# Kernel tuning notes

Hardware: AMD Instinct MI355X
Metric: run time of the kernel (lower is better)

Reference implementation:

```python
import jax, jax.numpy as jnp
import numpy as np

B, Q, HID = 2, 2048, 2048
HQ, HKV, D = 16, 4, 128
EPS = 1e-6
THETA = 1000000.0


def _rmsnorm(x, w):
    # x: [..., D]
    return x * jax.lax.rsqrt(jnp.mean(x * x, axis=-1, keepdims=True) + EPS) * w


def _rope(x, cos, sin):
    # neox-style: split halves. x: [B,Q,H,D], cos/sin: [B,Q,1,D/2]
    d2 = x.shape[-1] // 2
    x1, x2 = x[..., :d2], x[..., d2:]
    return jnp.concatenate([x1 * cos - x2 * sin, x2 * cos + x1 * sin], axis=-1)


def setup_inputs() -> dict:
    key = jax.random.key(0)
    k1, k2, k3 = jax.random.split(key, 3)
    positions = jnp.broadcast_to(jnp.arange(Q, dtype=jnp.int32), (B, Q))
    hidden_states = jax.random.normal(k1, (B, Q, HID), dtype=jnp.float32)
    k_cache = jnp.zeros((B, HKV, Q, D), dtype=jnp.float32)
    v_cache = jnp.zeros((B, HKV, Q, D), dtype=jnp.float32)
    wqkv = jax.random.normal(k2, (HQ * D + 2 * HKV * D, HID), dtype=jnp.float32) * (HID ** -0.5)
    wo = jax.random.normal(k3, (HID, HQ * D), dtype=jnp.float32) * ((HQ * D) ** -0.5)
    q_norm_w = jnp.ones((D,), dtype=jnp.float32)
    k_norm_w = jnp.ones((D,), dtype=jnp.float32)
    return {"positions": positions, "hidden_states": hidden_states, "k_cache": k_cache,
            "v_cache": v_cache, "wqkv": wqkv, "wo": wo, "q_norm_w": q_norm_w,
            "k_norm_w": k_norm_w, "seq_len": Q}


def reference(positions, hidden_states, k_cache, v_cache, wqkv, wo, q_norm_w, k_norm_w, seq_len):
    bsz, qlen, _ = hidden_states.shape
    q_size, kv_size = HQ * D, HKV * D
    scale = D ** -0.5

    qkv = hidden_states.reshape(bsz * qlen, HID) @ wqkv.T  # [B*Q, q+2kv]
    q = qkv[:, :q_size].reshape(bsz, qlen, HQ, D)
    k = qkv[:, q_size:q_size + kv_size].reshape(bsz, qlen, HKV, D)
    v = qkv[:, q_size + kv_size:].reshape(bsz, qlen, HKV, D)

    q = _rmsnorm(q, q_norm_w)
    k = _rmsnorm(k, k_norm_w)

    inv_freq = 1.0 / (THETA ** (jnp.arange(0, D, 2, dtype=jnp.float32) / D))  # [D/2]
    freqs = positions.astype(jnp.float32)[..., None] * inv_freq  # [B,Q,D/2]
    cos = jnp.cos(freqs)[:, :, None, :]
    sin = jnp.sin(freqs)[:, :, None, :]
    q = _rope(q, cos, sin)
    k = _rope(k, cos, sin)

    q = q.transpose(0, 2, 1, 3)  # [B,HQ,Q,D]
    k = k.transpose(0, 2, 1, 3)  # [B,HKV,Q,D]
    v = v.transpose(0, 2, 1, 3)

    start = seq_len - qlen
    k_cache = jax.lax.dynamic_update_slice(k_cache, k, (0, 0, start, 0))
    v_cache = jax.lax.dynamic_update_slice(v_cache, v, (0, 0, start, 0))
    k_full = k_cache[:, :, :seq_len, :]
    v_full = v_cache[:, :, :seq_len, :]

    rep = HQ // HKV
    kf = jnp.repeat(k_full, rep, axis=1)  # [B,HQ,S,D]
    vf = jnp.repeat(v_full, rep, axis=1)

    scores = jnp.einsum('bhqd,bhkd->bhqk', q, kf) * scale
    if qlen == seq_len:  # is_causal path
        causal = jnp.tril(jnp.ones((qlen, seq_len), dtype=bool))
        scores = jnp.where(causal, scores, jnp.finfo(scores.dtype).min)
    attn = jax.nn.softmax(scores, axis=-1)
    out = jnp.einsum('bhqk,bhkd->bhqd', attn, vf)  # [B,HQ,Q,D]
    out = out.transpose(0, 2, 1, 3).reshape(bsz * qlen, HQ * D)
    return (out @ wo.T).reshape(bsz, qlen, HID)
```

## Files before the change

### kernel.cpp

```cpp
#include <hip/hip_runtime.h>

#define B_    2
#define Q_    2048
#define HID_  2048
#define HQ_   16
#define HKV_  4
#define D_    128
#define QSC_  (0.08838834764831843f * 1.4426950408889634f)
#define LOG2_THETA 19.931568569324174f
#define FMAX_ 20.0f

typedef unsigned short u16;
typedef __attribute__((ext_vector_type(8))) short bf16x8;
typedef __attribute__((ext_vector_type(4))) float f32x4;

__device__ __forceinline__ u16 f2bf(float x) {
  union { float f; unsigned int u; } v; v.f = x;
  unsigned int r = v.u + 0x7FFFu + ((v.u >> 16) & 1u);
  return (u16)(r >> 16);
}
__device__ __forceinline__ u16 f2bf_t(float x) {
  union { float f; unsigned int u; } v; v.f = x;
  return (u16)(v.u >> 16);
}

__device__ __forceinline__ void gl2lds16(u16* lds, const u16* g) {
  __builtin_amdgcn_global_load_lds((const __attribute__((address_space(1))) void*)g,
                                   (__attribute__((address_space(3))) void*)lds,
                                   16, 0, 0);
}

#define N4_HID  2097152
#define N4_WQKV 1572864
#define N4_WO   1048576
#define N4_ALL  (N4_HID + N4_WQKV + N4_WO)
#define NROPE   (B_ * Q_ * 64)
__global__ __launch_bounds__(256) void cvt_all(const float* __restrict__ h,
                                               const float* __restrict__ wq,
                                               const float* __restrict__ wo,
                                               const int* __restrict__ pos,
                                               u16* __restrict__ oh,
                                               u16* __restrict__ owq,
                                               u16* __restrict__ owo,
                                               float* __restrict__ rope) {
  int i = blockIdx.x * 256 + threadIdx.x;
  if (i >= N4_ALL) {
    int j = i - N4_ALL;
    int d = j & 63, row = j >> 6;
    float p = (float)pos[row];
    float inv = exp2f(-(float)d * (LOG2_THETA / 64.f));
    float sn, cn;
    sincosf(p * inv, &sn, &cn);
    ((float2*)rope)[j] = make_float2(cn, sn);
    return;
  }
  const float* src; u16* dst; int off;
  if (i < N4_HID)                 { src = h;  dst = oh;  off = i; }
  else if (i < N4_HID + N4_WQKV)  { src = wq; dst = owq; off = i - N4_HID; }
  else                            { src = wo; dst = owo; off = i - N4_HID - N4_WQKV; }
  float4 v = *(const float4*)(src + (size_t)off * 4);
  ushort4 o;
  o.x = f2bf(v.x); o.y = f2bf(v.y); o.z = f2bf(v.z); o.w = f2bf(v.w);
  *(ushort4*)(dst + (size_t)off * 4) = o;
}

__global__ __launch_bounds__(256) void gemm_qkv(const u16* __restrict__ A,
                                                const u16* __restrict__ Bw,
                                                const float* __restrict__ rope,
                                                const float* __restrict__ qw,
                                                const float* __restrict__ kw,
                                                u16* __restrict__ qb,
                                                u16* __restrict__ kb,
                                                u16* __restrict__ vt) {
  __shared__ __align__(16) u16 lds[12288];
  u16* As = lds;
  u16* Bs = lds + 4096;
  const int tid = threadIdx.x;
  const int wv = tid >> 6, lane = tid & 63;
  const int c = lane & 15, quad = lane >> 4;
  const int lr = lane >> 2, lp = lane & 3;
  const int lpg = (lp + 4 - ((lr >> 1) & 3)) & 3;
  const int swq = ((quad + (c >> 1)) & 3) * 8;
  const int m0 = blockIdx.x * 128;
  const int by = blockIdx.y;
  const int n0 = by * 128;
  f32x4 acc[2][8] = {};
  for (int k0 = 0; k0 < HID_; k0 += 32) {
    __syncthreads();
#pragma unroll
    for (int i = 0; i < 2; i++) {
      int r = wv * 16 + i * 64 + lr;
      gl2lds16(As + (size_t)(wv * 64 + i * 256) * 8,
               A + (size_t)(m0 + r) * HID_ + k0 + lpg * 8);
      gl2lds16(Bs + (size_t)(wv * 64 + i * 256) * 8,
               Bw + (size_t)(n0 + r) * HID_ + k0 + lpg * 8);
    }
    __syncthreads();
    bf16x8 af[2], bfr[8];
#pragma unroll
    for (int mi = 0; mi < 2; mi++)
      af[mi] = *(const bf16x8*)(As + (wv * 32 + mi * 16 + c) * 32 + swq);
#pragma unroll
    for (int ni = 0; ni < 8; ni++)
      bfr[ni] = *(const bf16x8*)(Bs + (ni * 16 + c) * 32 + swq);
#pragma unroll
    for (int mi = 0; mi < 2; mi++)
#pragma unroll
      for (int ni = 0; ni < 8; ni++)
        acc[mi][ni] = __builtin_amdgcn_mfma_f32_16x16x32_bf16(af[mi], bfr[ni],
                                                              acc[mi][ni], 0, 0, 0);
  }
  __syncthreads();

  if (by < 20) {
    const bool isq = by < 16;
    const float* w = isq ? qw : kw;
    const float osc = isq ? QSC_ : 1.f;
    float wl[8];
#pragma unroll
    for (int ni = 0; ni < 8; ni++) wl[ni] = w[ni * 16 + c];
    u16* dstbuf = isq ? qb : kb;
    const int hbase = isq ? by : (by - 16);
    const int nheads = isq ? HQ_ : HKV_;
#pragma unroll
    for (int ph = 0; ph < 2; ph++) {
      if (ph) __syncthreads();
      if ((wv >> 1) == ph) {
#pragma unroll
        for (int mi = 0; mi < 2; mi++)
#pragma unroll
          for (int r = 0; r < 4; r++) {
            const int row = m0 + wv * 32 + mi * 16 + quad * 4 + r;
            const int q = row & (Q_ - 1), b = row >> 11;
            float ss = 0.f;
#pragma unroll
            for (int ni = 0; ni < 8; ni++) ss += acc[mi][ni][r] * acc[mi][ni][r];
            ss += __shfl_xor(ss, 1); ss += __shfl_xor(ss, 2);
            ss += __shfl_xor(ss, 4); ss += __shfl_xor(ss, 8);
            const float rn = rsqrtf(ss * (1.f / 128.f) + 1e-6f) * osc;
            u16* lrow = lds + ((wv & 1) * 32 + mi * 16 + quad * 4 + r) * 132;
#pragma unroll
            for (int ni = 0; ni < 4; ni++) {
              float2 cssn = *(const float2*)(rope +
                  ((size_t)(b * Q_ + q) * 64 + ni * 16 + c) * 2);
              float x1 = acc[mi][ni][r]     * wl[ni]     * rn;
              float x2 = acc[mi][ni + 4][r] * wl[ni + 4] * rn;
              lrow[ni * 16 + c]       = f2bf(x1 * cssn.x - x2 * cssn.y);
              lrow[(ni + 4) * 16 + c] = f2bf(x2 * cssn.x + x1 * cssn.y);
            }
          }
      }
      __syncthreads();
      const int rowg = m0 + ph * 64 + (tid >> 2);
      const int q = rowg & (Q_ - 1), b = rowg >> 11;
      u16* dst = dstbuf + (((size_t)(b * nheads) + hbase) * Q_ + q) * D_ + (tid & 3) * 32;
      const u16* srcl = lds + (tid >> 2) * 132 + (tid & 3) * 32;
#pragma unroll
      for (int j = 0; j < 4; j++)
        *(bf16x8*)(dst + j * 8) = *(const bf16x8*)(srcl + j * 8);
    }
  } else {
    const int hk = by - 20;
    const int bb = m0 >> 11, q0 = m0 & (Q_ - 1);
    u16* vw = lds + wv * 3072;
#pragma unroll
    for (int mi = 0; mi < 2; mi++) {
      if (mi) __syncthreads();
#pragma unroll
      for (int ni = 0; ni < 8; ni++) {
        short4 pv;
        pv.x = (short)f2bf(acc[mi][ni][0]); pv.y = (short)f2bf(acc[mi][ni][1]);
        pv.z = (short)f2bf(acc[mi][ni][2]); pv.w = (short)f2bf(acc[mi][ni][3]);
        *(short4*)(vw + (ni * 16 + c) * 24 + quad * 4) = pv;
      }
      __syncthreads();
#pragma unroll
      for (int it = 0; it < 2; it++) {
        const int d = it * 64 + lane;
        const u16* src = vw + d * 24;
        u16* dst = vt + (((size_t)(bb * HKV_) + hk) * D_ + d) * Q_ +
                   q0 + wv * 32 + mi * 16;
        *(bf16x8*)(dst)     = *(const bf16x8*)(src);
        *(bf16x8*)(dst + 8) = *(const bf16x8*)(src + 8);
      }
    }
  }
}

__global__ __launch_bounds__(256) void gemm_bt(const u16* __restrict__ A,
                                               const u16* __restrict__ Bw,
                                               float* __restrict__ C,
                                               int M, int N, int K) {
  __shared__ __align__(16) u16 As[128 * 32];
  __shared__ __align__(16) u16 Bs[128 * 32];
  const int tid = threadIdx.x;
  const int wave = tid >> 6, lane = tid & 63;
  const int wm = wave & 1, wn = wave >> 1;
  const int row16 = lane & 15, quad = lane >> 4;
  const int lr = lane >> 2, lp = lane & 3;
  const int lpg = (lp + 4 - ((lr >> 1) & 3)) & 3;
  const int swq = ((quad + (row16 >> 1)) & 3) * 8;
  const int m0 = blockIdx.x * 128, n0 = blockIdx.y * 128;
  f32x4 acc[4][4] = {};
  for (int k0 = 0; k0 < K; k0 += 32) {
    __syncthreads();
#pragma unroll
    for (int i = 0; i < 2; i++) {
      int r = wave * 16 + i * 64 + lr;
      gl2lds16(As + (size_t)(wave * 64 + i * 256) * 8,
               A + (size_t)(m0 + r) * K + k0 + lpg * 8);
      gl2lds16(Bs + (size_t)(wave * 64 + i * 256) * 8,
               Bw + (size_t)(n0 + r) * K + k0 + lpg * 8);
    }
    __syncthreads();
    bf16x8 af[4], bfr[4];
#pragma unroll
    for (int t = 0; t < 4; t++) {
      af[t]  = *(const bf16x8*)(As + (wm * 64 + t * 16 + row16) * 32 + swq);
      bfr[t] = *(const bf16x8*)(Bs + (wn * 64 + t * 16 + row16) * 32 + swq);
    }
#pragma unroll
    for (int mi = 0; mi < 4; mi++)
#pragma unroll
      for (int ni = 0; ni < 4; ni++)
        acc[mi][ni] = __builtin_amdgcn_mfma_f32_16x16x32_bf16(af[mi], bfr[ni],
                                                              acc[mi][ni], 0, 0, 0);
  }
#pragma unroll
  for (int mi = 0; mi < 4; mi++) {
    int row = m0 + wm * 64 + mi * 16 + quad * 4;
#pragma unroll
    for (int ni = 0; ni < 4; ni++) {
      int col = n0 + wn * 64 + ni * 16 + row16;
#pragma unroll
      for (int r = 0; r < 4; r++)
        C[(size_t)(row + r) * N + col] = acc[mi][ni][r];
    }
  }
}

__global__ __launch_bounds__(256) void attn_fwd(const u16* __restrict__ qb,
                                                const u16* __restrict__ kb,
                                                const u16* __restrict__ vt,
                                                u16* __restrict__ ob) {
  __shared__ __align__(16) u16 lds[8192 + 8192 + 4608];
  u16* Ks = lds;
  u16* Vs = lds + 8192;
  u16* Ps = lds + 16384;
  const int p = blockIdx.x, h = blockIdx.y, b = blockIdx.z;
  const int hk = h >> 2;
  const int tid = threadIdx.x, wave = tid >> 6, lane = tid & 63;
  const int c = lane & 15, quad = lane >> 4;
  const int lr = lane >> 2, lp = lane & 3;
  const int lpg = (lp + 4 - ((lr >> 1) & 3)) & 3;
  const int swq = ((quad + (c >> 1)) & 3) * 8;
  const u16* qg = qb + ((size_t)b * HQ_ + h) * (size_t)Q_ * D_;
  const u16* kg = kb + ((size_t)b * HKV_ + hk) * (size_t)Q_ * D_;
  const u16* vg = vt + ((size_t)b * HKV_ + hk) * (size_t)D_ * Q_;
  u16* Pw = Ps + wave * 1152;
  u16* Bw = Ks + wave * 2176;

#pragma unroll 1
  for (int tp = 0; tp < 2; tp++) {
    const int t = tp ? (31 - p) : p;
    const int q0 = t * 64;
    const int qrow = q0 + wave * 16 + c;
    bf16x8 qf[4];
#pragma unroll
    for (int kk = 0; kk < 4; kk++)
      qf[kk] = *(const bf16x8*)(qg + (size_t)qrow * D_ + kk * 32 + quad * 8);
    f32x4 Oa[8] = {};
    float l_acc = 0.f;

#pragma unroll 1
    for (int kt = 0; kt <= t; kt++) {
      __syncthreads();
#pragma unroll
      for (int i = 0; i < 4; i++) {
        gl2lds16(Ks + (size_t)(i * 256 + wave * 64) * 8,
                 kg + ((size_t)kt * 64 + wave * 16 + lr) * D_ + i * 32 + lpg * 8);
        int d = (i & 1) * 64 + wave * 16 + lr;
        gl2lds16(Vs + (size_t)(i * 256 + wave * 64) * 8,
                 vg + (size_t)d * Q_ + kt * 64 + (i >> 1) * 32 + lpg * 8);
      }
      __syncthreads();
      f32x4 S[4];
#pragma unroll
      for (int n = 0; n < 4; n++) {
        f32x4 a = {-FMAX_, -FMAX_, -FMAX_, -FMAX_};
#pragma unroll
        for (int kk = 0; kk < 4; kk++) {
          bf16x8 kf = *(const bf16x8*)(Ks + kk * 2048 + (n * 16 + c) * 32 + swq);
          a = __builtin_amdgcn_mfma_f32_16x16x32_bf16(kf, qf[kk], a, 0, 0, 0);
        }
        S[n] = a;
      }
      if (kt == t) {
#pragma unroll
        for (int n = 0; n < 4; n++)
#pragma unroll
          for (int r = 0; r < 4; r++) {
            int key = kt * 64 + n * 16 + quad * 4 + r;
            if (key > qrow) S[n][r] = -1e9f;
          }
      }
#pragma unroll
      for (int n = 0; n < 4; n++) {
        float p0 = __builtin_amdgcn_exp2f(S[n][0]);
        float p1 = __builtin_amdgcn_exp2f(S[n][1]);
        float p2 = __builtin_amdgcn_exp2f(S[n][2]);
        float p3 = __builtin_amdgcn_exp2f(S[n][3]);
        l_acc += (p0 + p1) + (p2 + p3);
        short4 pk;
        pk.x = (short)f2bf_t(p0); pk.y = (short)f2bf_t(p1);
        pk.z = (short)f2bf_t(p2); pk.w = (short)f2bf_t(p3);
        *(short4*)(Pw + c * 72 + n * 16 + quad * 4) = pk;
      }
      bf16x8 pf[2];
#pragma unroll
      for (int kk2 = 0; kk2 < 2; kk2++)
        pf[kk2] = *(const bf16x8*)(Pw + c * 72 + kk2 * 32 + quad * 8);
#pragma unroll
      for (int md = 0; md < 8; md++)
#pragma unroll
        for (int kk2 = 0; kk2 < 2; kk2++) {
          bf16x8 vf = *(const bf16x8*)(Vs + kk2 * 4096 + (md * 16 + c) * 32 + swq);
          Oa[md] = __builtin_amdgcn_mfma_f32_16x16x32_bf16(vf, pf[kk2], Oa[md], 0, 0, 0);
        }
    }
    float l_row = l_acc;
    l_row += __shfl_xor(l_row, 16);
    l_row += __shfl_xor(l_row, 32);
    __syncthreads();
    const float invl = 1.f / l_row;
#pragma unroll
    for (int md = 0; md < 8; md++) {
      short4 ok;
      ok.x = (short)f2bf(Oa[md][0] * invl); ok.y = (short)f2bf(Oa[md][1] * invl);
      ok.z = (short)f2bf(Oa[md][2] * invl); ok.w = (short)f2bf(Oa[md][3] * invl);
      *(short4*)(Bw + c * 136 + md * 16 + quad * 4) = ok;
    }
    const int orow = q0 + wave * 16 + lr;
#pragma unroll
    for (int tt = 0; tt < 4; tt++) {
      bf16x8 ov = *(const bf16x8*)(Bw + lr * 136 + lp * 32 + tt * 8);
      *(bf16x8*)(ob + ((size_t)(b * Q_ + orow) * HQ_ + h) * D_ + lp * 32 + tt * 8) = ov;
    }
  }
}

extern "C" void kernel_launch(void* const* d_in, const int* in_sizes, int n_in,
                              void* d_out, int out_size, void* d_ws, size_t ws_size,
                              hipStream_t stream) {
  const int*   positions = (const int*)  d_in[0];
  const float* hidden    = (const float*)d_in[1];
  const float* wqkv      = (const float*)d_in[4];
  const float* wo        = (const float*)d_in[5];
  const float* qnw       = (const float*)d_in[6];
  const float* knw       = (const float*)d_in[7];
  char* ws = (char*)d_ws;
  u16*   hid_bf  = (u16*)(ws);
  u16*   wqkv_bf = (u16*)(ws + 16777216);
  u16*   wo_bf   = (u16*)(ws + 29360128);
  u16*   q_bf    = (u16*)(ws + 37748736);
  u16*   k_bf    = (u16*)(ws + 54525952);
  u16*   vt_bf   = (u16*)(ws + 58720256);
  float* rope    = (float*)(ws + 62914560);
  u16*   attn_bf = hid_bf;

  cvt_all<<<19456, 256, 0, stream>>>(hidden, wqkv, wo, positions,
                                     hid_bf, wqkv_bf, wo_bf, rope);
  gemm_qkv<<<dim3(32, 24), 256, 0, stream>>>(hid_bf, wqkv_bf, rope, qnw, knw,
                                             q_bf, k_bf, vt_bf);
  attn_fwd<<<dim3(16, 16, 2), 256, 0, stream>>>(q_bf, k_bf, vt_bf, attn_bf);
  gemm_bt<<<dim3(32, 16), 256, 0, stream>>>(attn_bf, wo_bf, (float*)d_out, 4096, 2048, 2048);
}
```

Measured before the change: 338.9 us.

## Rewrite output projection GEMM with 256x256 tiles and pipelined LDS staging

```diff
diff --git a/kernel.cpp b/kernel.cpp
--- a/kernel.cpp
+++ b/kernel.cpp
@@ -187,56 +187,195 @@
   }
 }
 
-__global__ __launch_bounds__(256) void gemm_bt(const u16* __restrict__ A,
-                                               const u16* __restrict__ Bw,
-                                               float* __restrict__ C,
-                                               int M, int N, int K) {
-  __shared__ __align__(16) u16 As[128 * 32];
-  __shared__ __align__(16) u16 Bs[128 * 32];
+__global__ __launch_bounds__(512) void gemm_bt8(const u16* __restrict__ A,
+                                                const u16* __restrict__ Bw,
+                                                float* __restrict__ C,
+                                                int M, int N, int K) {
+  __shared__ __align__(16) u16 lds[65536];
   const int tid = threadIdx.x;
-  const int wave = tid >> 6, lane = tid & 63;
-  const int wm = wave & 1, wn = wave >> 1;
-  const int row16 = lane & 15, quad = lane >> 4;
-  const int lr = lane >> 2, lp = lane & 3;
-  const int lpg = (lp + 4 - ((lr >> 1) & 3)) & 3;
-  const int swq = ((quad + (row16 >> 1)) & 3) * 8;
-  const int m0 = blockIdx.x * 128, n0 = blockIdx.y * 128;
-  f32x4 acc[4][4] = {};
-  for (int k0 = 0; k0 < K; k0 += 32) {
-    __syncthreads();
-#pragma unroll
-    for (int i = 0; i < 2; i++) {
-      int r = wave * 16 + i * 64 + lr;
-      gl2lds16(As + (size_t)(wave * 64 + i * 256) * 8,
-               A + (size_t)(m0 + r) * K + k0 + lpg * 8);
-      gl2lds16(Bs + (size_t)(wave * 64 + i * 256) * 8,
-               Bw + (size_t)(n0 + r) * K + k0 + lpg * 8);
-    }
-    __syncthreads();
-    bf16x8 af[4], bfr[4];
-#pragma unroll
-    for (int t = 0; t < 4; t++) {
-      af[t]  = *(const bf16x8*)(As + (wm * 64 + t * 16 + row16) * 32 + swq);
-      bfr[t] = *(const bf16x8*)(Bs + (wn * 64 + t * 16 + row16) * 32 + swq);
-    }
-#pragma unroll
-    for (int mi = 0; mi < 4; mi++)
-#pragma unroll
-      for (int ni = 0; ni < 4; ni++)
-        acc[mi][ni] = __builtin_amdgcn_mfma_f32_16x16x32_bf16(af[mi], bfr[ni],
-                                                              acc[mi][ni], 0, 0, 0);
+  const int wv = tid >> 6, lane = tid & 63;
+  const int wm = wv >> 2, wn = wv & 3;
+  const int c = lane & 15, quad = lane >> 4;
+  const int m0 = blockIdx.x * 256, n0 = blockIdx.y * 256;
+  const int xg = ((lane & 7) ^ (lane >> 3)) * 8;
+  const int x0 = ((quad)     ^ (c & 7)) * 8;
+  const int x1 = ((quad | 4) ^ (c & 7)) * 8;
+  const int aoff = wm * 8192 + c * 64;
+  const int boff = 32768 + (wn >> 1) * 8192 + (wn & 1) * 4096 + c * 64;
+  const u16* Ag = A  + (size_t)m0 * K;
+  const u16* Bg = Bw + (size_t)n0 * K;
+  const int NIT = K >> 7;
+
+#define STG8(base, g, h, kt, buf)                                             \
+  { _Pragma("unroll")                                                         \
+    for (int j = 0; j < 2; ++j) {                                             \
+      const int s = j * 8 + wv;                                               \
+      gl2lds16(lds + (base) + (buf) * 16384 + (h) * 8192 + s * 512,           \
+               (g) + (size_t)((h) * 128 + s * 8 + (lane >> 3)) * K            \
+                   + (kt) * 64 + xg);                                         \
+    } }
+#define STG_A8(h, kt, buf) STG8(0,     Ag, h, kt, buf)
+#define STG_B8(h, kt, buf) STG8(32768, Bg, h, kt, buf)
+#define BAR8()  asm volatile("s_barrier" ::: "memory")
+#define WLG8()  { asm volatile("s_waitcnt lgkmcnt(0)" ::: "memory");          \
+                  __builtin_amdgcn_sched_barrier(0); }
+#define WVM8(n) { asm volatile("s_waitcnt vmcnt(" #n ")" ::: "memory");       \
+                  __builtin_amdgcn_sched_barrier(0); }
+#define MFMA8(MF, NF, KS) acc[MF][NF] = __builtin_amdgcn_mfma_f32_16x16x32_bf16( \
+                  fA[(MF) & 3][KS], fB[NF][KS], acc[MF][NF], 0, 0, 0)
+
+  f32x4 acc[8][4] = {};
+  bf16x8 fA[4][2], fB[4][2];
+
+  STG_A8(0, 0, 0); STG_A8(1, 0, 0); STG_B8(0, 0, 0); STG_B8(1, 0, 0);
+  STG_B8(0, 1, 1); STG_A8(0, 1, 1);
+  WVM8(4);
+  BAR8();
+
+#pragma unroll 1
+  for (int it = 0; it < NIT; ++it) {
+    const bool last = (it == NIT - 1);
+    const int kt1 = 2 * it + 1, kt2 = 2 * it + 2, kt3 = 2 * it + 3;
+
+#pragma unroll
+    for (int mf = 0; mf < 4; ++mf) {
+      fA[mf][0] = *(const bf16x8*)(lds + aoff + mf * 1024 + x0);
+      fA[mf][1] = *(const bf16x8*)(lds + aoff + mf * 1024 + x1);
+    }
+#pragma unroll
+    for (int nf = 0; nf < 2; ++nf) {
+      fB[nf][0] = *(const bf16x8*)(lds + boff + nf * 1024 + x0);
+      fB[nf][1] = *(const bf16x8*)(lds + boff + nf * 1024 + x1);
+    }
+    STG_A8(1, kt1, 1);
+    BAR8(); WLG8();
+    __builtin_amdgcn_s_setprio(1);
+#pragma unroll
+    for (int mf = 0; mf < 4; ++mf)
+#pragma unroll
+      for (int nf = 0; nf < 2; ++nf) { MFMA8(mf, nf, 0); MFMA8(mf, nf, 1); }
+    __builtin_amdgcn_s_setprio(0);
+    BAR8();
+
+#pragma unroll
+    for (int nf = 2; nf < 4; ++nf) {
+      fB[nf][0] = *(const bf16x8*)(lds + boff + nf * 1024 + x0);
+      fB[nf][1] = *(const bf16x8*)(lds + boff + nf * 1024 + x1);
+    }
+    STG_B8(1, kt1, 1);
+    BAR8(); WLG8();
+    __builtin_amdgcn_s_setprio(1);
+#pragma unroll
+    for (int mf = 0; mf < 4; ++mf)
+#pragma unroll
+      for (int nf = 2; nf < 4; ++nf) { MFMA8(mf, nf, 0); MFMA8(mf, nf, 1); }
+    __builtin_amdgcn_s_setprio(0);
+    BAR8();
+
+#pragma unroll
+    for (int mf = 0; mf < 4; ++mf) {
+      fA[mf][0] = *(const bf16x8*)(lds + aoff + (4 + mf) * 1024 + x0);
+      fA[mf][1] = *(const bf16x8*)(lds + aoff + (4 + mf) * 1024 + x1);
+    }
+    if (!last) STG_B8(0, kt2, 0);
+    BAR8(); WLG8();
+    __builtin_amdgcn_s_setprio(1);
+#pragma unroll
+    for (int mf = 4; mf < 8; ++mf)
+#pragma unroll
+      for (int nf = 2; nf < 4; ++nf) { MFMA8(mf, nf, 0); MFMA8(mf, nf, 1); }
+    __builtin_amdgcn_s_setprio(0);
+    BAR8();
+
+    if (!last) STG_A8(0, kt2, 0);
+    BAR8(); WLG8();
+    __builtin_amdgcn_s_setprio(1);
+#pragma unroll
+    for (int mf = 4; mf < 8; ++mf)
+#pragma unroll
+      for (int nf = 0; nf < 2; ++nf) { MFMA8(mf, nf, 0); MFMA8(mf, nf, 1); }
+    __builtin_amdgcn_s_setprio(0);
+    if (last) { WVM8(0); } else { WVM8(4); }
+    BAR8();
+
+#pragma unroll
+    for (int mf = 0; mf < 4; ++mf) {
+      fA[mf][0] = *(const bf16x8*)(lds + 16384 + aoff + mf * 1024 + x0);
+      fA[mf][1] = *(const bf16x8*)(lds + 16384 + aoff + mf * 1024 + x1);
+    }
+#pragma unroll
+    for (int nf = 0; nf < 2; ++nf) {
+      fB[nf][0] = *(const bf16x8*)(lds + 16384 + boff + nf * 1024 + x0);
+      fB[nf][1] = *(const bf16x8*)(lds + 16384 + boff + nf * 1024 + x1);
+    }
+    if (!last) STG_A8(1, kt2, 0);
+    BAR8(); WLG8();
+    __builtin_amdgcn_s_setprio(1);
+#pragma unroll
+    for (int mf = 0; mf < 4; ++mf)
+#pragma unroll
+      for (int nf = 0; nf < 2; ++nf) { MFMA8(mf, nf, 0); MFMA8(mf, nf, 1); }
+    __builtin_amdgcn_s_setprio(0);
+    BAR8();
+
+#pragma unroll
+    for (int nf = 2; nf < 4; ++nf) {
+      fB[nf][0] = *(const bf16x8*)(lds + 16384 + boff + nf * 1024 + x0);
+      fB[nf][1] = *(const bf16x8*)(lds + 16384 + boff + nf * 1024 + x1);
+    }
+    if (!last) STG_B8(1, kt2, 0);
+    BAR8(); WLG8();
+    __builtin_amdgcn_s_setprio(1);
+#pragma unroll
+    for (int mf = 0; mf < 4; ++mf)
+#pragma unroll
+      for (int nf = 2; nf < 4; ++nf) { MFMA8(mf, nf, 0); MFMA8(mf, nf, 1); }
+    __builtin_amdgcn_s_setprio(0);
+    BAR8();
+
+#pragma unroll
+    for (int mf = 0; mf < 4; ++mf) {
+      fA[mf][0] = *(const bf16x8*)(lds + 16384 + aoff + (4 + mf) * 1024 + x0);
+      fA[mf][1] = *(const bf16x8*)(lds + 16384 + aoff + (4 + mf) * 1024 + x1);
+    }
+    if (!last) STG_B8(0, kt3, 1);
+    BAR8(); WLG8();
+    __builtin_amdgcn_s_setprio(1);
+#pragma unroll
+    for (int mf = 4; mf < 8; ++mf)
+#pragma unroll
+      for (int nf = 2; nf < 4; ++nf) { MFMA8(mf, nf, 0); MFMA8(mf, nf, 1); }
+    __builtin_amdgcn_s_setprio(0);
+    BAR8();
+
+    if (!last) STG_A8(0, kt3, 1);
+    BAR8(); WLG8();
+    __builtin_amdgcn_s_setprio(1);
+#pragma unroll
+    for (int mf = 4; mf < 8; ++mf)
+#pragma unroll
+      for (int nf = 0; nf < 2; ++nf) { MFMA8(mf, nf, 0); MFMA8(mf, nf, 1); }
+    __builtin_amdgcn_s_setprio(0);
+    if (last) { WVM8(0); } else { WVM8(4); }
+    BAR8();
   }
-#pragma unroll
-  for (int mi = 0; mi < 4; mi++) {
-    int row = m0 + wm * 64 + mi * 16 + quad * 4;
-#pragma unroll
-    for (int ni = 0; ni < 4; ni++) {
-      int col = n0 + wn * 64 + ni * 16 + row16;
-#pragma unroll
-      for (int r = 0; r < 4; r++)
-        C[(size_t)(row + r) * N + col] = acc[mi][ni][r];
-    }
-  }
+
+  const int crow = m0 + wm * 128 + quad * 4;
+  const int ccol = n0 + wn * 64 + c;
+#pragma unroll
+  for (int mf = 0; mf < 8; ++mf)
+#pragma unroll
+    for (int nf = 0; nf < 4; ++nf)
+#pragma unroll
+      for (int r = 0; r < 4; ++r)
+        C[(size_t)(crow + mf * 16 + r) * N + ccol + nf * 16] = acc[mf][nf][r];
+#undef STG8
+#undef STG_A8
+#undef STG_B8
+#undef BAR8
+#undef WLG8
+#undef WVM8
+#undef MFMA8
 }
 
 __global__ __launch_bounds__(256) void attn_fwd(const u16* __restrict__ qb,
@@ -373,5 +512,6 @@
   gemm_qkv<<<dim3(32, 24), 256, 0, stream>>>(hid_bf, wqkv_bf, rope, qnw, knw,
                                              q_bf, k_bf, vt_bf);
   attn_fwd<<<dim3(16, 16, 2), 256, 0, stream>>>(q_bf, k_bf, vt_bf, attn_bf);
-  gemm_bt<<<dim3(32, 16), 256, 0, stream>>>(attn_bf, wo_bf, (float*)d_out, 4096, 2048, 2048);
-}
+  gemm_bt8<<<dim3(16, 8), 512, 0, stream>>>(attn_bf, wo_bf, (float*)d_out,
+                                            4096, 2048, 2048);
+}
```

New measurement: 336.8 us. No clear change (-0.6%).
